# Kernel optimization log

Hardware: AMD Instinct MI355X
Metric: run time of the kernel (lower is better)

The kernel has to match this reference:

```python
import jax, jax.numpy as jnp
import numpy as np

N_PTS = 262144      # 512x512 coordinate grid
N_HEADS = 16
HID = 256
N_HID_LAYERS = 3
IN_F = 2
OUT_F = 3
PE_L = 10                  # NeRF positional-encoding frequencies
PE_DIM = 2 * IN_F * PE_L   # sin+cos per freq per coord = 40
CAP = N_PTS // N_HEADS     # balanced partition: points per head


def positional_encoding(x):
    # x: [..., IN_F] -> [..., PE_DIM]
    freqs = (2.0 ** jnp.arange(PE_L, dtype=x.dtype)) * jnp.pi          # [L]
    ang = x[..., None, :] * freqs[:, None]                              # [..., L, IN_F]
    pe = jnp.concatenate([jnp.sin(ang), jnp.cos(ang)], axis=-1)        # [..., L, 2*IN_F]
    return pe.reshape(*x.shape[:-1], PE_DIM)


def setup_inputs() -> dict:
    key = jax.random.key(0)
    ks = jax.random.split(key, 5)
    # Balanced random segment map (equivalent to the module's segment_weight),
    # converted to the static routing table the torch loop recomputes each step:
    # head_idx[h] = where(segment_weight == h)
    rng = np.random.default_rng(0)
    seg = rng.permutation(np.arange(N_PTS) % N_HEADS)
    head_idx = np.stack([np.where(seg == h)[0] for h in range(N_HEADS)]).astype(np.int32)  # [H, CAP]

    coords = jax.random.uniform(ks[0], (1, N_PTS, IN_F), minval=-1.0, maxval=1.0)

    def he(k, shape, fan_in):
        return jax.random.normal(k, shape, dtype=jnp.float32) * np.float32(np.sqrt(2.0 / fan_in))

    W_in = he(ks[1], (N_HEADS, PE_DIM, HID), PE_DIM)
    b_in = jnp.zeros((N_HEADS, HID), jnp.float32)
    W_hid = he(ks[2], (N_HEADS, N_HID_LAYERS, HID, HID), HID)
    b_hid = jnp.zeros((N_HEADS, N_HID_LAYERS, HID), jnp.float32)
    W_out = he(ks[3], (N_HEADS, HID, OUT_F), HID)
    b_out = jnp.zeros((N_HEADS, OUT_F), jnp.float32)

    return dict(coords=coords, head_idx=jnp.asarray(head_idx),
                W_in=W_in, b_in=b_in, W_hid=W_hid, b_hid=b_hid,
                W_out=W_out, b_out=b_out)


def reference(coords, head_idx, W_in, b_in, W_hid, b_hid, W_out, b_out):
    # --- dispatch: gather each head's points (torch: coords[:, index, :]) ---
    coords_h = coords[0][head_idx]                                      # [H, CAP, IN_F]
    # --- per-head MLP (relu_MLP with positional embedding) ---
    h = jax.nn.relu(jnp.einsum('hcd,hdf->hcf', positional_encoding(coords_h), W_in)
                    + b_in[:, None, :])                                 # [H, CAP, HID]
    for l in range(N_HID_LAYERS):
        h = jax.nn.relu(jnp.einsum('hcf,hfg->hcg', h, W_hid[:, l])
                        + b_hid[:, l, None, :])
    out_h = jnp.einsum('hcf,hfo->hco', h, W_out) + b_out[:, None, :]    # [H, CAP, OUT_F]
    # --- combine: scatter per-head outputs back (torch: output_final[0, index, :] = out) ---
    out_final = jnp.zeros((1, N_PTS, OUT_F), coords.dtype)
    out_final = out_final.at[0, head_idx.reshape(-1)].set(out_h.reshape(-1, OUT_F))
    return (out_final, coords)
```

## Files before the change

### kernel.cpp

```cpp
#include <hip/hip_runtime.h>

typedef unsigned short u16;
typedef unsigned int   u32;
typedef __bf16  bf16x8 __attribute__((ext_vector_type(8)));
typedef float   f32x16 __attribute__((ext_vector_type(16)));

#define CAP      16384
#define L0_ELS   (256*56)
#define HID_ELS  (256*256)
#define OUT_ELS  (32*256)
#define HEAD_WS  (L0_ELS + 3*HID_ELS + OUT_ELS)
#define HID_OFF  L0_ELS
#define OUT_OFF  (L0_ELS + 3*HID_ELS)

union F8 { u32 u[4]; bf16x8 v; };

__device__ __forceinline__ u16 f2b(float f) {
  u32 u = __float_as_uint(f); u += 0x7fffu + ((u >> 16) & 1u); return (u16)(u >> 16);
}
__device__ __forceinline__ u32 packbf2(float a, float b) {
  u32 ua = __float_as_uint(a); ua += 0x7fffu + ((ua >> 16) & 1u);
  u32 ub = __float_as_uint(b); ub += 0x7fffu + ((ub >> 16) & 1u);
  return (ua >> 16) | (ub & 0xffff0000u);
}

__device__ __forceinline__ f32x16 mfma16(bf16x8 a, bf16x8 b, f32x16 c) {
  return __builtin_amdgcn_mfma_f32_32x32x16_bf16(a, b, c, 0, 0, 0);
}

__device__ __forceinline__ void stage_now(const u16* g, short* l, int bytes, int tid) {
  for (int base = tid * 16; base < bytes; base += 8192)
    *(uint4*)((char*)l + base) = *(const uint4*)((const char*)g + base);
}
__device__ __forceinline__ void stage_ld(const u16* g, int bytes, int tid, uint4 st[4]) {
#pragma unroll
  for (int r = 0; r < 4; ++r) {
    const int base = tid * 16 + r * 8192;
    if (base < bytes) st[r] = *(const uint4*)((const char*)g + base);
  }
}
__device__ __forceinline__ void stage_st(short* l, int bytes, int tid, const uint4 st[4]) {
#pragma unroll
  for (int r = 0; r < 4; ++r) {
    const int base = tid * 16 + r * 8192;
    if (base < bytes) *(uint4*)((char*)l + base) = st[r];
  }
}

__device__ __forceinline__ bf16x8 fragL0(const short* sl, int i, int t, int n, int hh) {
  return *(const bf16x8*)((const char*)sl + (32*i + n)*112 + (2*t + hh)*16);
}
__device__ __forceinline__ bf16x8 fragH(const short* sl, int i, int t, int n, int hh) {
  return *(const bf16x8*)((const char*)sl + ((32*i + n) << 9) + (((2*t + hh) ^ (n & 7)) << 4));
}

__device__ __forceinline__ void load_bias_raw(const float* b, int r, int hh, float4 o[4]) {
#pragma unroll
  for (int g = 0; g < 4; ++g) o[g] = *(const float4*)(b + 32*r + 8*g + 4*hh);
}
__device__ __forceinline__ f32x16 bias_to_acc(const float4 raw[4]) {
  f32x16 a;
#pragma unroll
  for (int g = 0; g < 4; ++g) {
    a[4*g+0] = raw[g].x; a[4*g+1] = raw[g].y;
    a[4*g+2] = raw[g].z; a[4*g+3] = raw[g].w;
  }
  return a;
}

__device__ __forceinline__ void epilogue(f32x16 c, int hh, F8& t0, F8& t1) {
  u32 P[8];
#pragma unroll
  for (int i = 0; i < 8; ++i)
    P[i] = packbf2(fmaxf(c[2*i], 0.f), fmaxf(c[2*i+1], 0.f));
  u32 s0 = hh ? P[0] : P[2], s1 = hh ? P[1] : P[3];
  u32 s2 = hh ? P[4] : P[6], s3 = hh ? P[5] : P[7];
  u32 x0 = __shfl_xor(s0, 32, 64), x1 = __shfl_xor(s1, 32, 64);
  u32 x2 = __shfl_xor(s2, 32, 64), x3 = __shfl_xor(s3, 32, 64);
  t0.u[0] = hh ? x0 : P[0]; t0.u[1] = hh ? x1 : P[1];
  t0.u[2] = hh ? P[2] : x0; t0.u[3] = hh ? P[3] : x1;
  t1.u[0] = hh ? x2 : P[4]; t1.u[1] = hh ? x3 : P[5];
  t1.u[2] = hh ? P[6] : x2; t1.u[3] = hh ? P[7] : x3;
}

__global__ void prep(const float* __restrict__ W_in, const float* __restrict__ b_in,
                     const float* __restrict__ W_hid, const float* __restrict__ W_out,
                     u16* __restrict__ ws) {
  const int ct = blockIdx.x * 256 + threadIdx.x;
  const int head = ct / 27392;
  const int r = ct - head * 27392;
  u16 v[8]; int dst;
  if (r < 1792) {
    const int nn = r / 7, k0 = (r % 7) * 8;
#pragma unroll
    for (int j = 0; j < 8; ++j) {
      const int k = k0 + j;
      v[j] = (k < 40) ? f2b(W_in[head*10240 + k*256 + nn])
           : (k == 40) ? f2b(b_in[head*256 + nn]) : (u16)0;
    }
    dst = head*HEAD_WS + nn*56 + k0;
  } else if (r < 26368) {
    const int q = r - 1792, l = q >> 13, q2 = q & 8191;
    const int nn = q2 >> 5, cc = q2 & 31, kb = 8 * (cc ^ (nn & 7));
#pragma unroll
    for (int j = 0; j < 8; ++j)
      v[j] = f2b(W_hid[head*196608 + l*65536 + (kb + j)*256 + nn]);
    dst = head*HEAD_WS + HID_OFF + l*65536 + nn*256 + cc*8;
  } else {
    const int q = r - 26368;
    const int nn = q >> 5, cc = q & 31, kb = 8 * (cc ^ (nn & 7));
#pragma unroll
    for (int j = 0; j < 8; ++j)
      v[j] = (nn < 3) ? f2b(W_out[head*768 + (kb + j)*3 + nn]) : (u16)0;
    dst = head*HEAD_WS + OUT_OFF + nn*256 + cc*8;
  }
  uint4 o;
  o.x = (u32)v[0] | ((u32)v[1] << 16); o.y = (u32)v[2] | ((u32)v[3] << 16);
  o.z = (u32)v[4] | ((u32)v[5] << 16); o.w = (u32)v[6] | ((u32)v[7] << 16);
  *(uint4*)(ws + dst) = o;
}

__global__ void copy_coords(const uint4* __restrict__ s, uint4* __restrict__ d) {
  const int i = blockIdx.x * 256 + threadIdx.x;
  d[i] = s[i];
}

__launch_bounds__(512, 2)
__global__ void mlp_main(const float* __restrict__ coords, const int* __restrict__ head_idx,
                         const float* __restrict__ b_hid, const float* __restrict__ b_out,
                         const u16* __restrict__ ws, float* __restrict__ out) {
  __shared__ short ring[2 * 16384];
  const int tid = threadIdx.x;
  const int lane = tid & 63, wv = tid >> 6;
  const int n = lane & 31, hh = lane >> 5;
  const int head = blockIdx.x & 15, chunk = blockIdx.x >> 4;
  const u16* wsh = ws + head * HEAD_WS;

  stage_now(wsh + 0*3584, ring,          7168, tid);
  stage_now(wsh + 1*3584, ring + 16384,  7168, tid);

  const int pt = chunk*256 + wv*32 + n;
  const int g  = head_idx[head*CAP + pt];
  const float2 cxy = *(const float2*)(coords + 2*g);
  const float xs = cxy.x, ys = cxy.y;
  const float bo0 = b_out[head*3+0], bo1 = b_out[head*3+1], bo2 = b_out[head*3+2];

  F8 pe[3];
#pragma unroll
  for (int t = 0; t < 3; ++t) {
    float e[8];
#pragma unroll
    for (int half = 0; half < 2; ++half) {
      const int l = 4*t + 2*hh + half;
      if (l < 10) {
        const float fr = 3.14159265358979323846f * (float)(1 << l);
        float s1, c1, s2, c2;
        sincosf(xs * fr, &s1, &c1);
        sincosf(ys * fr, &s2, &c2);
        e[4*half+0] = s1; e[4*half+1] = s2; e[4*half+2] = c1; e[4*half+3] = c2;
      } else {
        e[4*half+0] = (l == 10) ? 1.0f : 0.0f;
        e[4*half+1] = 0.f; e[4*half+2] = 0.f; e[4*half+3] = 0.f;
      }
    }
    pe[t].u[0] = packbf2(e[0], e[1]); pe[t].u[1] = packbf2(e[2], e[3]);
    pe[t].u[2] = packbf2(e[4], e[5]); pe[t].u[3] = packbf2(e[6], e[7]);
  }

  F8 act0[16], act1[16];
  __syncthreads();

#pragma unroll
  for (int rp = 0; rp < 4; ++rp) {
    short* sl = ring + (rp & 1) * 16384;
    f32x16 acc0 = (f32x16)0.f, acc1 = (f32x16)0.f;
#pragma unroll
    for (int t = 0; t < 3; ++t) {
      acc0 = mfma16(fragL0(sl, 0, t, n, hh), pe[t].v, acc0);
      acc1 = mfma16(fragL0(sl, 1, t, n, hh), pe[t].v, acc1);
    }
    __syncthreads();
    const u16* src = (rp < 2) ? (wsh + (rp + 2)*3584) : (wsh + HID_OFF + (rp - 2)*16384);
    const int bytes = (rp < 2) ? 7168 : 32768;
    uint4 st[4];
    stage_ld(src, bytes, tid, st);
    epilogue(acc0, hh, act0[4*rp+0], act0[4*rp+1]);
    epilogue(acc1, hh, act0[4*rp+2], act0[4*rp+3]);
    stage_st(sl, bytes, tid, st);
  }

  auto hid_layer = [&](const float* bias, F8 (&ain)[16], F8 (&aout)[16],
                       const u16* j0, const u16* j1, const u16* j2, const u16* j3,
                       int b2, int b3) {
    float4 bc0[4], bc1[4], bn0[4], bn1[4];
    load_bias_raw(bias, 0, hh, bc0); load_bias_raw(bias, 1, hh, bc1);
    const u16* jsrc[4] = { j0, j1, j2, j3 };
    const int  jb[4]   = { 32768, 32768, b2, b3 };
#pragma unroll
    for (int rp = 0; rp < 4; ++rp) {
      short* sl = ring + (rp & 1) * 16384;
      if (rp < 3) { load_bias_raw(bias, 2*rp+2, hh, bn0); load_bias_raw(bias, 2*rp+3, hh, bn1); }
      f32x16 acc0 = bias_to_acc(bc0);
      f32x16 acc1 = bias_to_acc(bc1);
#pragma unroll
      for (int t = 0; t < 16; ++t) {
        bf16x8 a0 = fragH(sl, 0, t, n, hh);
        bf16x8 a1 = fragH(sl, 1, t, n, hh);
        acc0 = mfma16(a0, ain[t].v, acc0);
        acc1 = mfma16(a1, ain[t].v, acc1);
      }
      __syncthreads();
      uint4 st[4];
      if (jb[rp] > 0) stage_ld(jsrc[rp], jb[rp], tid, st);
      epilogue(acc0, hh, aout[4*rp+0], aout[4*rp+1]);
      epilogue(acc1, hh, aout[4*rp+2], aout[4*rp+3]);
      if (jb[rp] > 0) stage_st(sl, jb[rp], tid, st);
      if (rp < 3) {
#pragma unroll
        for (int q = 0; q < 4; ++q) { bc0[q] = bn0[q]; bc1[q] = bn1[q]; }
      }
    }
  };

  const u16* hb = wsh + HID_OFF;
  hid_layer(b_hid + (head*3+0)*256, act0, act1,
            hb + 2*16384, hb + 3*16384, hb + HID_ELS, hb + HID_ELS + 16384, 32768, 32768);
  hid_layer(b_hid + (head*3+1)*256, act1, act0,
            hb + HID_ELS + 2*16384, hb + HID_ELS + 3*16384,
            hb + 2*HID_ELS, hb + 2*HID_ELS + 16384, 32768, 32768);
  hid_layer(b_hid + (head*3+2)*256, act0, act1,
            hb + 2*HID_ELS + 2*16384, hb + 2*HID_ELS + 3*16384,
            wsh + OUT_OFF, (const u16*)0, 16384, 0);

  f32x16 acc = (f32x16)0.f;
#pragma unroll
  for (int t = 0; t < 16; ++t)
    acc = mfma16(fragH(ring, 0, t, n, hh), act1[t].v, acc);
  if (hh == 0) {
    const long base = (long)g * 3;
    out[base + 0] = acc[0] + bo0;
    out[base + 1] = acc[1] + bo1;
    out[base + 2] = acc[2] + bo2;
  }
}

extern "C" void kernel_launch(void* const* d_in, const int* in_sizes, int n_in,
                              void* d_out, int out_size, void* d_ws, size_t ws_size,
                              hipStream_t stream) {
  const float* coords   = (const float*)d_in[0];
  const int*   head_idx = (const int*)d_in[1];
  const float* W_in     = (const float*)d_in[2];
  const float* b_in     = (const float*)d_in[3];
  const float* W_hid    = (const float*)d_in[4];
  const float* b_hid    = (const float*)d_in[5];
  const float* W_out    = (const float*)d_in[6];
  const float* b_out    = (const float*)d_in[7];
  float* out = (float*)d_out;
  u16*   ws  = (u16*)d_ws;
  if (ws_size < (size_t)HEAD_WS * 16 * sizeof(u16)) return;

  prep<<<dim3(1712), dim3(256), 0, stream>>>(W_in, b_in, W_hid, W_out, ws);
  copy_coords<<<dim3(512), dim3(256), 0, stream>>>((const uint4*)coords, (uint4*)(out + 786432));
  mlp_main<<<dim3(1024), dim3(512), 0, stream>>>(coords, head_idx, b_hid, b_out, ws, out);
}
```

Measured before the change: 225.1 us.

## Process two point groups per wave to reuse weight fragments across MFMAs

Each wave now computes 64 points (two 32-point groups) instead of 32, so every LDS weight fragment feeds two MFMAs. Blocks shrink to 256 threads at one block per SIMD set. The weight layout becomes k-major and unswizzled, the first-layer K padding drops from 56 to 48, and the hidden-layer bias moves from accumulator init into the epilogue. The hidden-weight prep uses an LDS transpose for coalesced reads, and the small weights go to a separate prep kernel. This raises register pressure (four activation arrays) and cuts occupancy. The unswizzled layout may also cause LDS bank conflicts.

Result: slower. 356.3 us (+58.3%).

```diff
diff --git a/kernel.cpp b/kernel.cpp
--- a/kernel.cpp
+++ b/kernel.cpp
@@ -6,9 +6,9 @@
 typedef float   f32x16 __attribute__((ext_vector_type(16)));
 
 #define CAP      16384
-#define L0_ELS   (256*56)
-#define HID_ELS  (256*256)
-#define OUT_ELS  (32*256)
+#define L0_ELS   (256*48)
+#define HID_ELS  65536
+#define OUT_ELS  8192
 #define HEAD_WS  (L0_ELS + 3*HID_ELS + OUT_ELS)
 #define HID_OFF  L0_ELS
 #define OUT_OFF  (L0_ELS + 3*HID_ELS)
@@ -23,56 +23,41 @@
   u32 ub = __float_as_uint(b); ub += 0x7fffu + ((ub >> 16) & 1u);
   return (ua >> 16) | (ub & 0xffff0000u);
 }
-
 __device__ __forceinline__ f32x16 mfma16(bf16x8 a, bf16x8 b, f32x16 c) {
   return __builtin_amdgcn_mfma_f32_32x32x16_bf16(a, b, c, 0, 0, 0);
 }
 
 __device__ __forceinline__ void stage_now(const u16* g, short* l, int bytes, int tid) {
-  for (int base = tid * 16; base < bytes; base += 8192)
+  for (int base = tid * 16; base < bytes; base += 4096)
     *(uint4*)((char*)l + base) = *(const uint4*)((const char*)g + base);
 }
-__device__ __forceinline__ void stage_ld(const u16* g, int bytes, int tid, uint4 st[4]) {
-#pragma unroll
-  for (int r = 0; r < 4; ++r) {
-    const int base = tid * 16 + r * 8192;
+__device__ __forceinline__ void stage_ld(const u16* g, int bytes, int tid, uint4 st[8]) {
+#pragma unroll
+  for (int r = 0; r < 8; ++r) {
+    const int base = tid * 16 + r * 4096;
     if (base < bytes) st[r] = *(const uint4*)((const char*)g + base);
   }
 }
-__device__ __forceinline__ void stage_st(short* l, int bytes, int tid, const uint4 st[4]) {
-#pragma unroll
-  for (int r = 0; r < 4; ++r) {
-    const int base = tid * 16 + r * 8192;
+__device__ __forceinline__ void stage_st(short* l, int bytes, int tid, const uint4 st[8]) {
+#pragma unroll
+  for (int r = 0; r < 8; ++r) {
+    const int base = tid * 16 + r * 4096;
     if (base < bytes) *(uint4*)((char*)l + base) = st[r];
   }
 }
 
-__device__ __forceinline__ bf16x8 fragL0(const short* sl, int i, int t, int n, int hh) {
-  return *(const bf16x8*)((const char*)sl + (32*i + n)*112 + (2*t + hh)*16);
-}
-__device__ __forceinline__ bf16x8 fragH(const short* sl, int i, int t, int n, int hh) {
-  return *(const bf16x8*)((const char*)sl + ((32*i + n) << 9) + (((2*t + hh) ^ (n & 7)) << 4));
-}
-
-__device__ __forceinline__ void load_bias_raw(const float* b, int r, int hh, float4 o[4]) {
-#pragma unroll
-  for (int g = 0; g < 4; ++g) o[g] = *(const float4*)(b + 32*r + 8*g + 4*hh);
-}
-__device__ __forceinline__ f32x16 bias_to_acc(const float4 raw[4]) {
-  f32x16 a;
-#pragma unroll
-  for (int g = 0; g < 4; ++g) {
-    a[4*g+0] = raw[g].x; a[4*g+1] = raw[g].y;
-    a[4*g+2] = raw[g].z; a[4*g+3] = raw[g].w;
-  }
-  return a;
-}
-
-__device__ __forceinline__ void epilogue(f32x16 c, int hh, F8& t0, F8& t1) {
+__device__ __forceinline__ bf16x8 frag64(const short* sl, int i, int t, int n, int hh) {
+  return *(const bf16x8*)((const char*)sl + ((((2*t + hh) << 6) + 32*i + n) << 4));
+}
+__device__ __forceinline__ bf16x8 fragO(const short* sl, int t, int n, int hh) {
+  return *(const bf16x8*)((const char*)sl + ((((2*t + hh) << 5) + n) << 4));
+}
+
+__device__ __forceinline__ void epi_core(const float cb[16], int hh, F8& t0, F8& t1) {
   u32 P[8];
 #pragma unroll
   for (int i = 0; i < 8; ++i)
-    P[i] = packbf2(fmaxf(c[2*i], 0.f), fmaxf(c[2*i+1], 0.f));
+    P[i] = packbf2(fmaxf(cb[2*i], 0.f), fmaxf(cb[2*i+1], 0.f));
   u32 s0 = hh ? P[0] : P[2], s1 = hh ? P[1] : P[3];
   u32 s2 = hh ? P[4] : P[6], s3 = hh ? P[5] : P[7];
   u32 x0 = __shfl_xor(s0, 32, 64), x1 = __shfl_xor(s1, 32, 64);
@@ -82,37 +67,71 @@
   t1.u[0] = hh ? x2 : P[4]; t1.u[1] = hh ? x3 : P[5];
   t1.u[2] = hh ? P[6] : x2; t1.u[3] = hh ? P[7] : x3;
 }
-
-__global__ void prep(const float* __restrict__ W_in, const float* __restrict__ b_in,
-                     const float* __restrict__ W_hid, const float* __restrict__ W_out,
-                     u16* __restrict__ ws) {
-  const int ct = blockIdx.x * 256 + threadIdx.x;
-  const int head = ct / 27392;
-  const int r = ct - head * 27392;
+__device__ __forceinline__ void epilogue(f32x16 c, int hh, F8& t0, F8& t1) {
+  float cb[16];
+#pragma unroll
+  for (int e = 0; e < 16; ++e) cb[e] = c[e];
+  epi_core(cb, hh, t0, t1);
+}
+__device__ __forceinline__ void epilogueB(f32x16 c, const float4 bb[4], int hh, F8& t0, F8& t1) {
+  float cb[16];
+#pragma unroll
+  for (int e = 0; e < 16; ++e) cb[e] = c[e] + ((const float*)bb)[e];
+  epi_core(cb, hh, t0, t1);
+}
+
+__global__ void prep_hid(const float* __restrict__ W_hid, u16* __restrict__ ws) {
+  __shared__ u16 tile[64 * 72];
+  const int b = blockIdx.x;
+  const int kband = b & 3, q = (b >> 2) & 3, l = (b >> 4) % 3, head = b / 48;
+  const int t = threadIdx.x;
+  const int kl = t >> 2, rg = t & 3;
+  const float* src = W_hid + (((head*3 + l)*256 + kband*64 + kl) << 8) + q*64 + rg*16;
+  u16* dt = &tile[kl*72 + rg*16];
+#pragma unroll
+  for (int m = 0; m < 4; ++m) {
+    float4 v = *(const float4*)(src + m*4);
+    ushort4 o; o.x = f2b(v.x); o.y = f2b(v.y); o.z = f2b(v.z); o.w = f2b(v.w);
+    *(ushort4*)(dt + m*4) = o;
+  }
+  __syncthreads();
+  u16* dbase = ws + head*HEAD_WS + HID_OFF + l*HID_ELS + q*16384 + (kband << 12);
+#pragma unroll
+  for (int p = 0; p < 2; ++p) {
+    const int idx = t + p*256;
+    const int cl = idx >> 6, rq = idx & 63;
+    u16 v8[8];
+#pragma unroll
+    for (int j = 0; j < 8; ++j) v8[j] = tile[(cl*8 + j)*72 + rq];
+    uint4 o;
+    o.x = (u32)v8[0] | ((u32)v8[1] << 16); o.y = (u32)v8[2] | ((u32)v8[3] << 16);
+    o.z = (u32)v8[4] | ((u32)v8[5] << 16); o.w = (u32)v8[6] | ((u32)v8[7] << 16);
+    *(uint4*)(dbase + ((cl << 6) + rq) * 8) = o;
+  }
+}
+
+__global__ void prep_small(const float* __restrict__ W_in, const float* __restrict__ b_in,
+                           const float* __restrict__ W_out, u16* __restrict__ ws) {
+  const int r = blockIdx.x * 256 + threadIdx.x;
+  const int head = r / 2560, f = r % 2560;
   u16 v[8]; int dst;
-  if (r < 1792) {
-    const int nn = r / 7, k0 = (r % 7) * 8;
+  if (f < 1536) {
+    const int q = f / 384, g = f % 384;
+    const int c = g >> 6, row = g & 63, nn = q*64 + row, k0 = c*8;
 #pragma unroll
     for (int j = 0; j < 8; ++j) {
       const int k = k0 + j;
-      v[j] = (k < 40) ? f2b(W_in[head*10240 + k*256 + nn])
-           : (k == 40) ? f2b(b_in[head*256 + nn]) : (u16)0;
-    }
-    dst = head*HEAD_WS + nn*56 + k0;
-  } else if (r < 26368) {
-    const int q = r - 1792, l = q >> 13, q2 = q & 8191;
-    const int nn = q2 >> 5, cc = q2 & 31, kb = 8 * (cc ^ (nn & 7));
+      v[j] = (k < 40) ? f2b(W_in[head*10240 + (k << 8) + nn])
+           : (k == 40) ? f2b(b_in[(head << 8) + nn]) : (u16)0;
+    }
+    dst = head*HEAD_WS + q*3072 + g*8;
+  } else {
+    const int f2 = f - 1536;
+    const int c = f2 >> 5, nn = f2 & 31, k0 = c*8;
 #pragma unroll
     for (int j = 0; j < 8; ++j)
-      v[j] = f2b(W_hid[head*196608 + l*65536 + (kb + j)*256 + nn]);
-    dst = head*HEAD_WS + HID_OFF + l*65536 + nn*256 + cc*8;
-  } else {
-    const int q = r - 26368;
-    const int nn = q >> 5, cc = q & 31, kb = 8 * (cc ^ (nn & 7));
-#pragma unroll
-    for (int j = 0; j < 8; ++j)
-      v[j] = (nn < 3) ? f2b(W_out[head*768 + (kb + j)*3 + nn]) : (u16)0;
-    dst = head*HEAD_WS + OUT_OFF + nn*256 + cc*8;
+      v[j] = (nn < 3) ? f2b(W_out[head*768 + (k0 + j)*3 + nn]) : (u16)0;
+    dst = head*HEAD_WS + OUT_OFF + f2*8;
   }
   uint4 o;
   o.x = (u32)v[0] | ((u32)v[1] << 16); o.y = (u32)v[2] | ((u32)v[3] << 16);
@@ -125,7 +144,7 @@
   d[i] = s[i];
 }
 
-__launch_bounds__(512, 2)
+__launch_bounds__(256, 1)
 __global__ void mlp_main(const float* __restrict__ coords, const int* __restrict__ head_idx,
                          const float* __restrict__ b_hid, const float* __restrict__ b_out,
                          const u16* __restrict__ ws, float* __restrict__ out) {
@@ -136,111 +155,124 @@
   const int head = blockIdx.x & 15, chunk = blockIdx.x >> 4;
   const u16* wsh = ws + head * HEAD_WS;
 
-  stage_now(wsh + 0*3584, ring,          7168, tid);
-  stage_now(wsh + 1*3584, ring + 16384,  7168, tid);
-
-  const int pt = chunk*256 + wv*32 + n;
-  const int g  = head_idx[head*CAP + pt];
-  const float2 cxy = *(const float2*)(coords + 2*g);
-  const float xs = cxy.x, ys = cxy.y;
+  stage_now(wsh + 0*3072, ring,          6144, tid);
+  stage_now(wsh + 1*3072, ring + 16384,  6144, tid);
+
+  const int ptA = chunk*256 + wv*64 + n, ptB = ptA + 32;
+  const int gA = head_idx[head*CAP + ptA];
+  const int gB = head_idx[head*CAP + ptB];
+  const float2 cA = *(const float2*)(coords + 2*gA);
+  const float2 cB = *(const float2*)(coords + 2*gB);
   const float bo0 = b_out[head*3+0], bo1 = b_out[head*3+1], bo2 = b_out[head*3+2];
 
-  F8 pe[3];
-#pragma unroll
-  for (int t = 0; t < 3; ++t) {
-    float e[8];
-#pragma unroll
-    for (int half = 0; half < 2; ++half) {
-      const int l = 4*t + 2*hh + half;
-      if (l < 10) {
-        const float fr = 3.14159265358979323846f * (float)(1 << l);
-        float s1, c1, s2, c2;
-        sincosf(xs * fr, &s1, &c1);
-        sincosf(ys * fr, &s2, &c2);
-        e[4*half+0] = s1; e[4*half+1] = s2; e[4*half+2] = c1; e[4*half+3] = c2;
-      } else {
-        e[4*half+0] = (l == 10) ? 1.0f : 0.0f;
-        e[4*half+1] = 0.f; e[4*half+2] = 0.f; e[4*half+3] = 0.f;
+  F8 peA[3], peB[3];
+#pragma unroll
+  for (int grp = 0; grp < 2; ++grp) {
+    const float xs = grp ? cB.x : cA.x, ys = grp ? cB.y : cA.y;
+    F8* pe = grp ? peB : peA;
+#pragma unroll
+    for (int t = 0; t < 3; ++t) {
+      float e[8];
+#pragma unroll
+      for (int half = 0; half < 2; ++half) {
+        const int l = 4*t + 2*hh + half;
+        if (l < 10) {
+          const float fr = 3.14159265358979323846f * (float)(1 << l);
+          float s1, c1, s2, c2;
+          sincosf(xs * fr, &s1, &c1);
+          sincosf(ys * fr, &s2, &c2);
+          e[4*half+0] = s1; e[4*half+1] = s2; e[4*half+2] = c1; e[4*half+3] = c2;
+        } else {
+          e[4*half+0] = (l == 10) ? 1.0f : 0.0f;
+          e[4*half+1] = 0.f; e[4*half+2] = 0.f; e[4*half+3] = 0.f;
+        }
       }
-    }
-    pe[t].u[0] = packbf2(e[0], e[1]); pe[t].u[1] = packbf2(e[2], e[3]);
-    pe[t].u[2] = packbf2(e[4], e[5]); pe[t].u[3] = packbf2(e[6], e[7]);
-  }
-
-  F8 act0[16], act1[16];
+      pe[t].u[0] = packbf2(e[0], e[1]); pe[t].u[1] = packbf2(e[2], e[3]);
+      pe[t].u[2] = packbf2(e[4], e[5]); pe[t].u[3] = packbf2(e[6], e[7]);
+    }
+  }
+
+  F8 actA0[16], actA1[16], actB0[16], actB1[16];
   __syncthreads();
 
 #pragma unroll
   for (int rp = 0; rp < 4; ++rp) {
     short* sl = ring + (rp & 1) * 16384;
-    f32x16 acc0 = (f32x16)0.f, acc1 = (f32x16)0.f;
+    f32x16 aA0 = (f32x16)0.f, aA1 = (f32x16)0.f, aB0 = (f32x16)0.f, aB1 = (f32x16)0.f;
 #pragma unroll
     for (int t = 0; t < 3; ++t) {
-      acc0 = mfma16(fragL0(sl, 0, t, n, hh), pe[t].v, acc0);
-      acc1 = mfma16(fragL0(sl, 1, t, n, hh), pe[t].v, acc1);
+      bf16x8 f0 = frag64(sl, 0, t, n, hh);
+      bf16x8 f1 = frag64(sl, 1, t, n, hh);
+      aA0 = mfma16(f0, peA[t].v, aA0); aB0 = mfma16(f0, peB[t].v, aB0);
+      aA1 = mfma16(f1, peA[t].v, aA1); aB1 = mfma16(f1, peB[t].v, aB1);
     }
     __syncthreads();
-    const u16* src = (rp < 2) ? (wsh + (rp + 2)*3584) : (wsh + HID_OFF + (rp - 2)*16384);
-    const int bytes = (rp < 2) ? 7168 : 32768;
-    uint4 st[4];
+    const u16* src = (rp < 2) ? (wsh + (rp + 2)*3072) : (wsh + HID_OFF + (rp - 2)*16384);
+    const int bytes = (rp < 2) ? 6144 : 32768;
+    uint4 st[8];
     stage_ld(src, bytes, tid, st);
-    epilogue(acc0, hh, act0[4*rp+0], act0[4*rp+1]);
-    epilogue(acc1, hh, act0[4*rp+2], act0[4*rp+3]);
+    epilogue(aA0, hh, actA0[4*rp+0], actA0[4*rp+1]);
+    epilogue(aA1, hh, actA0[4*rp+2], actA0[4*rp+3]);
+    epilogue(aB0, hh, actB0[4*rp+0], actB0[4*rp+1]);
+    epilogue(aB1, hh, actB0[4*rp+2], actB0[4*rp+3]);
     stage_st(sl, bytes, tid, st);
   }
 
-  auto hid_layer = [&](const float* bias, F8 (&ain)[16], F8 (&aout)[16],
+  auto hid_layer = [&](const float* bias, F8 (&ainA)[16], F8 (&ainB)[16],
+                       F8 (&aoutA)[16], F8 (&aoutB)[16],
                        const u16* j0, const u16* j1, const u16* j2, const u16* j3,
                        int b2, int b3) {
-    float4 bc0[4], bc1[4], bn0[4], bn1[4];
-    load_bias_raw(bias, 0, hh, bc0); load_bias_raw(bias, 1, hh, bc1);
     const u16* jsrc[4] = { j0, j1, j2, j3 };
     const int  jb[4]   = { 32768, 32768, b2, b3 };
 #pragma unroll
     for (int rp = 0; rp < 4; ++rp) {
       short* sl = ring + (rp & 1) * 16384;
-      if (rp < 3) { load_bias_raw(bias, 2*rp+2, hh, bn0); load_bias_raw(bias, 2*rp+3, hh, bn1); }
-      f32x16 acc0 = bias_to_acc(bc0);
-      f32x16 acc1 = bias_to_acc(bc1);
+      f32x16 aA0 = (f32x16)0.f, aA1 = (f32x16)0.f, aB0 = (f32x16)0.f, aB1 = (f32x16)0.f;
 #pragma unroll
       for (int t = 0; t < 16; ++t) {
-        bf16x8 a0 = fragH(sl, 0, t, n, hh);
-        bf16x8 a1 = fragH(sl, 1, t, n, hh);
-        acc0 = mfma16(a0, ain[t].v, acc0);
-        acc1 = mfma16(a1, ain[t].v, acc1);
+        bf16x8 f0 = frag64(sl, 0, t, n, hh);
+        bf16x8 f1 = frag64(sl, 1, t, n, hh);
+        aA0 = mfma16(f0, ainA[t].v, aA0); aB0 = mfma16(f0, ainB[t].v, aB0);
+        aA1 = mfma16(f1, ainA[t].v, aA1); aB1 = mfma16(f1, ainB[t].v, aB1);
       }
       __syncthreads();
-      uint4 st[4];
+      uint4 st[8];
       if (jb[rp] > 0) stage_ld(jsrc[rp], jb[rp], tid, st);
-      epilogue(acc0, hh, aout[4*rp+0], aout[4*rp+1]);
-      epilogue(acc1, hh, aout[4*rp+2], aout[4*rp+3]);
+      float4 bb0[4], bb1[4];
+#pragma unroll
+      for (int g2 = 0; g2 < 4; ++g2) {
+        bb0[g2] = *(const float4*)(bias + 64*rp +      8*g2 + 4*hh);
+        bb1[g2] = *(const float4*)(bias + 64*rp + 32 + 8*g2 + 4*hh);
+      }
+      epilogueB(aA0, bb0, hh, aoutA[4*rp+0], aoutA[4*rp+1]);
+      epilogueB(aA1, bb1, hh, aoutA[4*rp+2], aoutA[4*rp+3]);
+      epilogueB(aB0, bb0, hh, aoutB[4*rp+0], aoutB[4*rp+1]);
+      epilogueB(aB1, bb1, hh, aoutB[4*rp+2], aoutB[4*rp+3]);
       if (jb[rp] > 0) stage_st(sl, jb[rp], tid, st);
-      if (rp < 3) {
-#pragma unroll
-        for (int q = 0; q < 4; ++q) { bc0[q] = bn0[q]; bc1[q] = bn1[q]; }
-      }
     }
   };
 
   const u16* hb = wsh + HID_OFF;
-  hid_layer(b_hid + (head*3+0)*256, act0, act1,
+  hid_layer(b_hid + (head*3+0)*256, actA0, actB0, actA1, actB1,
             hb + 2*16384, hb + 3*16384, hb + HID_ELS, hb + HID_ELS + 16384, 32768, 32768);
-  hid_layer(b_hid + (head*3+1)*256, act1, act0,
+  hid_layer(b_hid + (head*3+1)*256, actA1, actB1, actA0, actB0,
             hb + HID_ELS + 2*16384, hb + HID_ELS + 3*16384,
             hb + 2*HID_ELS, hb + 2*HID_ELS + 16384, 32768, 32768);
-  hid_layer(b_hid + (head*3+2)*256, act0, act1,
+  hid_layer(b_hid + (head*3+2)*256, actA0, actB0, actA1, actB1,
             hb + 2*HID_ELS + 2*16384, hb + 2*HID_ELS + 3*16384,
             wsh + OUT_OFF, (const u16*)0, 16384, 0);
 
-  f32x16 acc = (f32x16)0.f;
-#pragma unroll
-  for (int t = 0; t < 16; ++t)
-    acc = mfma16(fragH(ring, 0, t, n, hh), act1[t].v, acc);
+  f32x16 oA = (f32x16)0.f, oB = (f32x16)0.f;
+#pragma unroll
+  for (int t = 0; t < 16; ++t) {
+    bf16x8 f = fragO(ring, t, n, hh);
+    oA = mfma16(f, actA1[t].v, oA);
+    oB = mfma16(f, actB1[t].v, oB);
+  }
   if (hh == 0) {
-    const long base = (long)g * 3;
-    out[base + 0] = acc[0] + bo0;
-    out[base + 1] = acc[1] + bo1;
-    out[base + 2] = acc[2] + bo2;
+    const long bA = (long)gA * 3, bB = (long)gB * 3;
+    out[bA + 0] = oA[0] + bo0; out[bA + 1] = oA[1] + bo1; out[bA + 2] = oA[2] + bo2;
+    out[bB + 0] = oB[0] + bo0; out[bB + 1] = oB[1] + bo1; out[bB + 2] = oB[2] + bo2;
   }
 }
 
@@ -259,7 +291,8 @@
   u16*   ws  = (u16*)d_ws;
   if (ws_size < (size_t)HEAD_WS * 16 * sizeof(u16)) return;
 
-  prep<<<dim3(1712), dim3(256), 0, stream>>>(W_in, b_in, W_hid, W_out, ws);
+  prep_hid  <<<dim3(768), dim3(256), 0, stream>>>(W_hid, ws);
+  prep_small<<<dim3(160), dim3(256), 0, stream>>>(W_in, b_in, W_out, ws);
   copy_coords<<<dim3(512), dim3(256), 0, stream>>>((const uint4*)coords, (uint4*)(out + 786432));
-  mlp_main<<<dim3(1024), dim3(512), 0, stream>>>(coords, head_idx, b_hid, b_out, ws, out);
-}
+  mlp_main  <<<dim3(1024), dim3(256), 0, stream>>>(coords, head_idx, b_hid, b_out, ws, out);
+}
```

## Transpose hidden weights via shared-memory tiles, fuse coords copy, hoist weight prefetch

Applied to the files above, without the earlier changes.

The prep kernel now converts W_hid through a 64x64 shared-memory transpose tile, so global reads are coalesced float4 loads instead of strided scalar gathers. The coords copy kernel is folded into prep to save one launch. In mlp_main, the global loads for the next weight slab are issued before the MFMA loop rather than after the barrier, so their latency overlaps compute at the cost of more live registers. packbf2 now uses the HIP bf16 conversion intrinsic.

New measurement: 266.0 us. 1.18x slower.

```diff
diff --git a/kernel.cpp b/kernel.cpp
--- a/kernel.cpp
+++ b/kernel.cpp
@@ -1,4 +1,5 @@
 #include <hip/hip_runtime.h>
+#include <hip/hip_bf16.h>
 
 typedef unsigned short u16;
 typedef unsigned int   u32;
@@ -7,8 +8,8 @@
 
 #define CAP      16384
 #define L0_ELS   (256*56)
-#define HID_ELS  (256*256)
-#define OUT_ELS  (32*256)
+#define HID_ELS  65536
+#define OUT_ELS  8192
 #define HEAD_WS  (L0_ELS + 3*HID_ELS + OUT_ELS)
 #define HID_OFF  L0_ELS
 #define OUT_OFF  (L0_ELS + 3*HID_ELS)
@@ -19,11 +20,9 @@
   u32 u = __float_as_uint(f); u += 0x7fffu + ((u >> 16) & 1u); return (u16)(u >> 16);
 }
 __device__ __forceinline__ u32 packbf2(float a, float b) {
-  u32 ua = __float_as_uint(a); ua += 0x7fffu + ((ua >> 16) & 1u);
-  u32 ub = __float_as_uint(b); ub += 0x7fffu + ((ub >> 16) & 1u);
-  return (ua >> 16) | (ub & 0xffff0000u);
-}
-
+  __hip_bfloat162 h = __float22bfloat162_rn(make_float2(a, b));
+  return *(u32*)&h;
+}
 __device__ __forceinline__ f32x16 mfma16(bf16x8 a, bf16x8 b, f32x16 c) {
   return __builtin_amdgcn_mfma_f32_32x32x16_bf16(a, b, c, 0, 0, 0);
 }
@@ -84,45 +83,70 @@
 }
 
 __global__ void prep(const float* __restrict__ W_in, const float* __restrict__ b_in,
-                     const float* __restrict__ W_hid, const float* __restrict__ W_out,
-                     u16* __restrict__ ws) {
-  const int ct = blockIdx.x * 256 + threadIdx.x;
-  const int head = ct / 27392;
-  const int r = ct - head * 27392;
+                     const float* __restrict__ W_hid, const float* __restrict__ b_in_unused,
+                     const float* __restrict__ W_out, u16* __restrict__ ws,
+                     const uint4* __restrict__ csrc, uint4* __restrict__ cdst) {
+  __shared__ u16 tile[64 * 72];
+  const int t = threadIdx.x;
+  if (blockIdx.x < 768) {
+    const int b = blockIdx.x;
+    const int kband = b & 3, q = (b >> 2) & 3, l = (b >> 4) % 3, head = b / 48;
+    const int kl = t >> 2, rg = t & 3;
+    const float* src = W_hid + (((head*3 + l)*256 + kband*64 + kl) << 8) + q*64 + rg*16;
+    u16* dt = &tile[kl*72 + rg*16];
+#pragma unroll
+    for (int m = 0; m < 4; ++m) {
+      float4 v = *(const float4*)(src + m*4);
+      ushort4 o; o.x = f2b(v.x); o.y = f2b(v.y); o.z = f2b(v.z); o.w = f2b(v.w);
+      *(ushort4*)(dt + m*4) = o;
+    }
+    __syncthreads();
+    u16* lbase = ws + head*HEAD_WS + HID_OFF + l*HID_ELS;
+#pragma unroll
+    for (int p = 0; p < 2; ++p) {
+      const int idx = t + p*256;
+      const int cl = idx >> 6, rq = idx & 63;
+      const int nn = q*64 + rq, cc = kband*8 + cl;
+      const int klc = (cl ^ (rq & 7)) * 8;
+      u16 v8[8];
+#pragma unroll
+      for (int j = 0; j < 8; ++j) v8[j] = tile[(klc + j)*72 + rq];
+      uint4 o;
+      o.x = (u32)v8[0] | ((u32)v8[1] << 16); o.y = (u32)v8[2] | ((u32)v8[3] << 16);
+      o.z = (u32)v8[4] | ((u32)v8[5] << 16); o.w = (u32)v8[6] | ((u32)v8[7] << 16);
+      *(uint4*)(lbase + (nn << 8) + cc*8) = o;
+    }
+    return;
+  }
+  if (blockIdx.x >= 944) {
+    const int i = (blockIdx.x - 944) * 256 + t;
+    cdst[i] = csrc[i];
+    return;
+  }
+  const int r = (blockIdx.x - 768) * 256 + t;
+  const int head = r / 2816, f = r % 2816;
   u16 v[8]; int dst;
-  if (r < 1792) {
-    const int nn = r / 7, k0 = (r % 7) * 8;
+  if (f < 1792) {
+    const int nn = f / 7, k0 = (f % 7) * 8;
 #pragma unroll
     for (int j = 0; j < 8; ++j) {
       const int k = k0 + j;
-      v[j] = (k < 40) ? f2b(W_in[head*10240 + k*256 + nn])
-           : (k == 40) ? f2b(b_in[head*256 + nn]) : (u16)0;
+      v[j] = (k < 40) ? f2b(W_in[head*10240 + (k << 8) + nn])
+           : (k == 40) ? f2b(b_in[(head << 8) + nn]) : (u16)0;
     }
     dst = head*HEAD_WS + nn*56 + k0;
-  } else if (r < 26368) {
-    const int q = r - 1792, l = q >> 13, q2 = q & 8191;
-    const int nn = q2 >> 5, cc = q2 & 31, kb = 8 * (cc ^ (nn & 7));
-#pragma unroll
-    for (int j = 0; j < 8; ++j)
-      v[j] = f2b(W_hid[head*196608 + l*65536 + (kb + j)*256 + nn]);
-    dst = head*HEAD_WS + HID_OFF + l*65536 + nn*256 + cc*8;
   } else {
-    const int q = r - 26368;
-    const int nn = q >> 5, cc = q & 31, kb = 8 * (cc ^ (nn & 7));
+    const int f2 = f - 1792;
+    const int nn = f2 >> 5, cc = f2 & 31, kb = 8 * (cc ^ (nn & 7));
 #pragma unroll
     for (int j = 0; j < 8; ++j)
       v[j] = (nn < 3) ? f2b(W_out[head*768 + (kb + j)*3 + nn]) : (u16)0;
-    dst = head*HEAD_WS + OUT_OFF + nn*256 + cc*8;
+    dst = head*HEAD_WS + OUT_OFF + (nn << 8) + cc*8;
   }
   uint4 o;
   o.x = (u32)v[0] | ((u32)v[1] << 16); o.y = (u32)v[2] | ((u32)v[3] << 16);
   o.z = (u32)v[4] | ((u32)v[5] << 16); o.w = (u32)v[6] | ((u32)v[7] << 16);
   *(uint4*)(ws + dst) = o;
-}
-
-__global__ void copy_coords(const uint4* __restrict__ s, uint4* __restrict__ d) {
-  const int i = blockIdx.x * 256 + threadIdx.x;
-  d[i] = s[i];
 }
 
 __launch_bounds__(512, 2)
@@ -135,6 +159,7 @@
   const int n = lane & 31, hh = lane >> 5;
   const int head = blockIdx.x & 15, chunk = blockIdx.x >> 4;
   const u16* wsh = ws + head * HEAD_WS;
+  const u16* hb  = wsh + HID_OFF;
 
   stage_now(wsh + 0*3584, ring,          7168, tid);
   stage_now(wsh + 1*3584, ring + 16384,  7168, tid);
@@ -173,6 +198,10 @@
 #pragma unroll
   for (int rp = 0; rp < 4; ++rp) {
     short* sl = ring + (rp & 1) * 16384;
+    const u16* src = (rp < 2) ? (wsh + (rp + 2)*3584) : (hb + (rp - 2)*16384);
+    const int bytes = (rp < 2) ? 7168 : 32768;
+    uint4 st[4];
+    stage_ld(src, bytes, tid, st);
     f32x16 acc0 = (f32x16)0.f, acc1 = (f32x16)0.f;
 #pragma unroll
     for (int t = 0; t < 3; ++t) {
@@ -180,10 +209,6 @@
       acc1 = mfma16(fragL0(sl, 1, t, n, hh), pe[t].v, acc1);
     }
     __syncthreads();
-    const u16* src = (rp < 2) ? (wsh + (rp + 2)*3584) : (wsh + HID_OFF + (rp - 2)*16384);
-    const int bytes = (rp < 2) ? 7168 : 32768;
-    uint4 st[4];
-    stage_ld(src, bytes, tid, st);
     epilogue(acc0, hh, act0[4*rp+0], act0[4*rp+1]);
     epilogue(acc1, hh, act0[4*rp+2], act0[4*rp+3]);
     stage_st(sl, bytes, tid, st);
@@ -200,6 +225,8 @@
     for (int rp = 0; rp < 4; ++rp) {
       short* sl = ring + (rp & 1) * 16384;
       if (rp < 3) { load_bias_raw(bias, 2*rp+2, hh, bn0); load_bias_raw(bias, 2*rp+3, hh, bn1); }
+      uint4 st[4];
+      if (jb[rp] > 0) stage_ld(jsrc[rp], jb[rp], tid, st);
       f32x16 acc0 = bias_to_acc(bc0);
       f32x16 acc1 = bias_to_acc(bc1);
 #pragma unroll
@@ -210,8 +237,6 @@
         acc1 = mfma16(a1, ain[t].v, acc1);
       }
       __syncthreads();
-      uint4 st[4];
-      if (jb[rp] > 0) stage_ld(jsrc[rp], jb[rp], tid, st);
       epilogue(acc0, hh, aout[4*rp+0], aout[4*rp+1]);
       epilogue(acc1, hh, aout[4*rp+2], aout[4*rp+3]);
       if (jb[rp] > 0) stage_st(sl, jb[rp], tid, st);
@@ -222,7 +247,6 @@
     }
   };
 
-  const u16* hb = wsh + HID_OFF;
   hid_layer(b_hid + (head*3+0)*256, act0, act1,
             hb + 2*16384, hb + 3*16384, hb + HID_ELS, hb + HID_ELS + 16384, 32768, 32768);
   hid_layer(b_hid + (head*3+1)*256, act1, act0,
@@ -259,7 +283,7 @@
   u16*   ws  = (u16*)d_ws;
   if (ws_size < (size_t)HEAD_WS * 16 * sizeof(u16)) return;
 
-  prep<<<dim3(1712), dim3(256), 0, stream>>>(W_in, b_in, W_hid, W_out, ws);
-  copy_coords<<<dim3(512), dim3(256), 0, stream>>>((const uint4*)coords, (uint4*)(out + 786432));
+  prep<<<dim3(1456), dim3(256), 0, stream>>>(W_in, b_in, W_hid, b_in, W_out, ws,
+                                             (const uint4*)coords, (uint4*)(out + 786432));
   mlp_main<<<dim3(1024), dim3(512), 0, stream>>>(coords, head_idx, b_hid, b_out, ws, out);
 }
```
